# Kernel tuning notes

Measured on AMD Instinct MI355X. Metric: run time of the kernel, lower is better.

The kernel has to match this reference:

```python
import jax, jax.numpy as jnp
import numpy as np
from jax import lax

# --- static dims (match init_kwargs) ---
B = 16
Y, M, WIN = 10, 12, 48          # input_years, months_per_year, num_windows_per_month
T = Y * M * WIN                  # 5760 encoder timesteps
DENC = 256                       # encoder hidden size
U = 128                          # att_single_dense_units (bahdanau dim)
A1, A2 = 64, 32                  # att_single_dense_1st/2nd
K = 8                            # monthly/yearly num_kernels
KS, MPOOL, YPOOL = 3, 2, 2       # kernel_size, pool sizes (strides=1, VALID)
AMY = 64                         # att_mon_year_dense_1st
RNN = 256                        # RNN_num_units
FDEC = 64                        # dec_input features
NOUT = 64                        # n_output_features
# conv/pool output sizes (VALID conv, VALID pool stride 1)
H1, W1 = WIN - KS + 1 - MPOOL + 1, U - KS + 1 - MPOOL + 1      # 45, 125
H2, W2 = H1 - KS + 1 - MPOOL + 1, W1 - KS + 1 - MPOOL + 1      # 42, 122
FLATM = H2 * W2 * K                                            # 40992
HY, WY = M * H1 - KS + 1 - YPOOL + 1, W1 - KS + 1 - YPOOL + 1  # 537, 122
FLATY = HY * WY * K                                            # 524112


def conv_tanh(x, k, b):
    # Keras Conv2D(valid, activation='tanh'), NHWC/HWIO
    y = lax.conv_general_dilated(x, k, (1, 1), 'VALID',
                                 dimension_numbers=('NHWC', 'HWIO', 'NHWC'))
    return jnp.tanh(y + b)


def maxpool(x, p):
    # MaxPooling2D(pool_size=p, strides=1, valid)
    return lax.reduce_window(x, -jnp.inf, lax.max, (1, p, p, 1), (1, 1, 1, 1), 'VALID')


def setup_inputs() -> dict:
    key = jax.random.key(0)
    ks = jax.random.split(key, 24)
    r = lambda i, shape, s=0.02: jax.random.normal(ks[i], shape, jnp.float32) * s
    return {
        'dec_input': jax.random.normal(ks[0], (B, 1, FDEC), jnp.float32),
        'S_prev_dec': jax.random.normal(ks[1], (B, RNN), jnp.float32),
        'C_prev_dec': jax.random.normal(ks[2], (B, RNN), jnp.float32),
        'h_enc': jax.random.normal(ks[3], (B, T, DENC), jnp.float32),
        # attention_single params (all use_bias=False)
        'W_enc': r(4, (DENC, U)), 'W_dec': r(5, (RNN, U)),
        'W_att1': r(6, (U, A1)), 'W_att2': r(7, (A1, A2)), 'W_att3': r(8, (A2, 1)),
        # conv_pool layers
        'conv1_k': r(9, (KS, KS, 1, K)), 'conv1_b': jnp.zeros((K,), jnp.float32),
        'conv2_k': r(10, (KS, KS, K, K)), 'conv2_b': jnp.zeros((K,), jnp.float32),
        'convy_k': r(11, (KS, KS, K, K)), 'convy_b': jnp.zeros((K,), jnp.float32),
        # monthly / yearly attention denses (use_bias=True)
        'Wm1': r(12, (FLATM, AMY)), 'bm1': jnp.zeros((AMY,), jnp.float32),
        'Wm2': r(13, (AMY, 1)), 'bm2': jnp.zeros((1,), jnp.float32),
        'Wy1': r(14, (FLATY, AMY)), 'by1': jnp.zeros((AMY,), jnp.float32),
        'Wy2': r(15, (AMY, 1)), 'by2': jnp.zeros((1,), jnp.float32),
        # LSTM (input dim = DENC + FDEC); gate order i,f,g,o as in Keras
        'W_lstm': r(16, (DENC + FDEC, 4 * RNN)), 'U_lstm': r(17, (RNN, 4 * RNN)),
        'b_lstm': jnp.zeros((4 * RNN,), jnp.float32),
        # output dense
        'W_out': r(18, (RNN, NOUT)), 'b_out': jnp.zeros((NOUT,), jnp.float32),
    }


def reference(dec_input, S_prev_dec, C_prev_dec, h_enc,
              W_enc, W_dec, W_att1, W_att2, W_att3,
              conv1_k, conv1_b, conv2_k, conv2_b, convy_k, convy_b,
              Wm1, bm1, Wm2, bm2, Wy1, by1, Wy2, by2,
              W_lstm, U_lstm, b_lstm, W_out, b_out):
    # --- Bahdanau additive attention over all T encoder steps ---
    bah = h_enc @ W_enc + (S_prev_dec @ W_dec)[:, None, :]          # [B,T,U]
    e = jax.nn.relu(jax.nn.relu(jnp.tanh(bah @ W_att1) @ W_att2) @ W_att3)  # [B,T,1]
    aw = jax.nn.softmax(e, axis=1)[..., 0]                          # [B,T]
    # --- monthly conv-pool attention, batched over all Y*M month slices ---
    x = bah.reshape(B * Y * M, WIN, U, 1)
    c1 = maxpool(conv_tanh(x, conv1_k, conv1_b), MPOOL)             # [BYM,H1,W1,K]
    c2 = maxpool(conv_tanh(c1, conv2_k, conv2_b), MPOOL)            # [BYM,H2,W2,K]
    em = jax.nn.relu(jnp.tanh(c2.reshape(B * Y * M, FLATM) @ Wm1 + bm1) @ Wm2 + bm2)
    m_att = jax.nn.softmax(em.reshape(B, Y, M), axis=2)             # softmax over months
    # --- yearly conv-pool attention (months concatenated along height) ---
    yin = c1.reshape(B * Y, M * H1, W1, K)
    cy = maxpool(conv_tanh(yin, convy_k, convy_b), YPOOL)           # [BY,HY,WY,K]
    ey = jax.nn.relu(jnp.tanh(cy.reshape(B * Y, FLATY) @ Wy1 + by1) @ Wy2 + by2)
    y_att = jax.nn.softmax(ey.reshape(B, Y), axis=1)                # softmax over years
    # --- hierarchical combination of weights ---
    new_w = (aw.reshape(B, Y, M, WIN) * m_att[..., None]
             * y_att[:, :, None, None]).reshape(B, T)               # [B,T]
    ctx = jnp.einsum('bt,btd->bd', new_w, h_enc)                    # context [B,DENC]
    # --- single LSTM step on [context ; dec_input] ---
    xt = jnp.concatenate([ctx[:, None, :], dec_input], axis=-1)[:, 0, :]
    z = xt @ W_lstm + S_prev_dec @ U_lstm + b_lstm
    i, f, g, o = jnp.split(z, 4, axis=-1)
    c_new = jax.nn.sigmoid(f) * C_prev_dec + jax.nn.sigmoid(i) * jnp.tanh(g)
    h_new = jax.nn.sigmoid(o) * jnp.tanh(c_new)
    out = jax.nn.relu(h_new[:, None, :] @ W_out + b_out)            # [B,1,NOUT]
    return out, h_new, c_new, new_w
```

## Files before the change

### kernel.cpp

```cpp
#include <hip/hip_runtime.h>
#include <hip/hip_bf16.h>

#define DEV static __device__ __forceinline__

#define B_    16
#define Y_    10
#define M_    12
#define WIN_  48
#define T_    5760
#define DENC_ 256
#define U_    128
#define A1_   64
#define A2_   32
#define K_    8
#define RNN_  256
#define FDEC_ 64
#define NOUT_ 64

#define H1_   45
#define W1_   125
#define H2_   42
#define W2_   122
#define FLATM_ 40992
#define HY_   537
#define WY_   122
#define FLATY_ 524112
#define NSM_  1920
#define NSY_  160

typedef __attribute__((ext_vector_type(8))) short s16x8;
typedef __attribute__((ext_vector_type(4))) short s16x4;
typedef __attribute__((ext_vector_type(4))) float f32x4;

DEV float rcpf(float x){ return __builtin_amdgcn_rcpf(x); }
DEV float tanh_fast(float x){
  x = fminf(fmaxf(x, -15.0f), 15.0f);
  float e = __expf(2.0f*x);
  return 1.0f - 2.0f*rcpf(e + 1.0f);
}
DEV float tanh_nc(float x){
  float e = __expf(2.0f*x);
  return 1.0f - 2.0f*rcpf(e + 1.0f);
}
DEV float sigm(float x){ return rcpf(1.0f + __expf(-x)); }
DEV float wredsum(float v){
  #pragma unroll
  for (int off=32; off; off>>=1) v += __shfl_xor(v, off, 64);
  return v;
}
DEV short f2b(float f){
  __hip_bfloat16 h = __float2bfloat16(f);
  return *reinterpret_cast<short*>(&h);
}
DEV float b2f(short s){
  unsigned int x = ((unsigned int)(unsigned short)s) << 16;
  return __uint_as_float(x);
}
DEV unsigned int cvt_pk_bf16(float lo, float hi){
  unsigned int r;
  asm("v_cvt_pk_bf16_f32 %0, %1, %2" : "=v"(r) : "v"(lo), "v"(hi));
  return r;
}
DEV unsigned int swz_xor1u(unsigned int v){
  return (unsigned int)__builtin_amdgcn_ds_swizzle((int)v, 0x041F);
}
DEV unsigned int permb(unsigned int hi_src, unsigned int lo_src, unsigned int sel){
  return __builtin_amdgcn_perm(hi_src, lo_src, sel);
}

__global__ void k_cvt_bf16(const float* __restrict__ src, short* __restrict__ dst, long n4){
  long i = (long)blockIdx.x*256 + threadIdx.x;
  if (i < n4){
    f32x4 v = *(const f32x4*)(src + i*4);
    s16x4 o;
    #pragma unroll
    for (int q=0;q<4;q++) o[q] = f2b(v[q]);
    *(s16x4*)(dst + i*4) = o;
  }
}

__global__ void k_sdec(const float* __restrict__ S, const float* __restrict__ Wd,
                       float* __restrict__ sdec){
  int b = blockIdx.x, u = threadIdx.x;
  const float* s = S + b*DENC_;
  float acc = 0.f;
  #pragma unroll 4
  for (int d=0; d<DENC_; d++) acc += s[d]*Wd[d*U_+u];
  sdec[b*U_+u] = acc;
}

__global__ __launch_bounds__(256)
void k_bah_mfma(const float* __restrict__ h_enc, const short* __restrict__ Wenc_bf,
                const float* __restrict__ sdec, short* __restrict__ bah16){
  __shared__ short Wl[128*136];
  int tid = threadIdx.x;
  int m0 = blockIdx.x * 64;
  int lane = tid & 63, wid = tid >> 6;
  int pl = lane & 15, g = lane >> 4;
  long arow = m0 + wid*16 + pl;
  const float* ap = h_enc + arow*DENC_;
  f32x4 acc[8];
  #pragma unroll
  for (int i=0;i<8;i++) acc[i] = (f32x4){0.f,0.f,0.f,0.f};

  for (int kh=0; kh<2; kh++){
    for (int i=tid; i<16384; i+=256){
      int k = i >> 7, c = i & 127;
      Wl[c*136 + k] = Wenc_bf[(kh*128 + k)*U_ + c];
    }
    __syncthreads();
    #pragma unroll
    for (int kk=0; kk<4; kk++){
      f32x4 a0 = *(const f32x4*)(ap + kh*128 + kk*32 + g*8);
      f32x4 a1 = *(const f32x4*)(ap + kh*128 + kk*32 + g*8 + 4);
      s16x8 a;
      #pragma unroll
      for (int q=0;q<4;q++){ a[q] = f2b(a0[q]); a[4+q] = f2b(a1[q]); }
      #pragma unroll
      for (int nt=0; nt<8; nt++){
        s16x8 b = *(const s16x8*)(Wl + (nt*16+pl)*136 + kk*32 + g*8);
        acc[nt] = __builtin_amdgcn_mfma_f32_16x16x32_bf16(a, b, acc[nt], 0,0,0);
      }
    }
    __syncthreads();
  }
  int b = m0 / T_;
  #pragma unroll
  for (int nt=0; nt<8; nt++){
    float sd = sdec[b*U_ + nt*16 + pl];
    #pragma unroll
    for (int q=0; q<4; q++){
      long r = m0 + wid*16 + g*4 + q;
      bah16[r*U_ + nt*16 + pl] = f2b(acc[nt][q] + sd);
    }
  }
}

__global__ __launch_bounds__(256)
void k_att_mfma(const short* __restrict__ bah16, const float* __restrict__ W1,
                const float* __restrict__ W2, const float* __restrict__ W3f,
                float* __restrict__ e_out){
  __shared__ short W1l[64*136];
  __shared__ short W2l[32*72];
  __shared__ float hl[64][68];
  __shared__ float w3s[32];
  int tid = threadIdx.x;
  int lane = tid & 63, wid = tid >> 6;
  int pl = lane & 15, g = lane >> 4;
  long m0 = (long)blockIdx.x * 64;

  for (int i=tid; i<8192; i+=256){ int k=i>>6, c=i&63; W1l[c*136+k] = f2b(W1[k*64+c]); }
  for (int i=tid; i<2048; i+=256){ int k=i>>5, c=i&31; W2l[c*72+k]  = f2b(W2[k*32+c]); }
  if (tid < 32) w3s[tid] = W3f[tid];
  __syncthreads();

  const short* Ab = bah16 + (m0 + wid*16 + pl)*U_;
  f32x4 acc1[4];
  #pragma unroll
  for (int i=0;i<4;i++) acc1[i]=(f32x4){0.f,0.f,0.f,0.f};
  #pragma unroll
  for (int kk=0; kk<4; kk++){
    s16x8 a = *(const s16x8*)(Ab + kk*32 + g*8);
    #pragma unroll
    for (int nt=0; nt<4; nt++){
      s16x8 b = *(const s16x8*)(&W1l[(nt*16+pl)*136 + kk*32 + g*8]);
      acc1[nt] = __builtin_amdgcn_mfma_f32_16x16x32_bf16(a, b, acc1[nt], 0,0,0);
    }
  }
  #pragma unroll
  for (int nt=0; nt<4; nt++)
    #pragma unroll
    for (int q=0; q<4; q++)
      hl[wid*16 + g*4 + q][nt*16 + pl] = tanh_fast(acc1[nt][q]);
  __syncthreads();

  f32x4 acc2[2];
  #pragma unroll
  for (int i=0;i<2;i++) acc2[i]=(f32x4){0.f,0.f,0.f,0.f};
  #pragma unroll
  for (int kk=0; kk<2; kk++){
    f32x4 h0 = *(const f32x4*)(&hl[wid*16+pl][kk*32 + g*8]);
    f32x4 h1 = *(const f32x4*)(&hl[wid*16+pl][kk*32 + g*8 + 4]);
    s16x8 a;
    #pragma unroll
    for (int q=0;q<4;q++){ a[q]=f2b(h0[q]); a[4+q]=f2b(h1[q]); }
    #pragma unroll
    for (int nt=0; nt<2; nt++){
      s16x8 b = *(const s16x8*)(&W2l[(nt*16+pl)*72 + kk*32 + g*8]);
      acc2[nt] = __builtin_amdgcn_mfma_f32_16x16x32_bf16(a, b, acc2[nt], 0,0,0);
    }
  }
  #pragma unroll
  for (int q=0; q<4; q++){
    float v = fmaxf(acc2[0][q],0.f)*w3s[pl] + fmaxf(acc2[1][q],0.f)*w3s[16+pl];
    #pragma unroll
    for (int off=1; off<16; off<<=1) v += __shfl_xor(v, off, 64);
    if (pl == 0) e_out[m0 + wid*16 + g*4 + q] = fmaxf(v, 0.f);
  }
}

__global__ __launch_bounds__(256)
void k_softmax(const float* __restrict__ e, float* __restrict__ aw){
  int b = blockIdx.x, tid = threadIdx.x;
  __shared__ float red[4];
  const float* eb = e + (long)b*T_;
  float m = -1e30f;
  for (int t=tid; t<T_; t+=256) m = fmaxf(m, eb[t]);
  #pragma unroll
  for (int off=32; off; off>>=1) m = fmaxf(m, __shfl_xor(m, off, 64));
  if ((tid&63)==0) red[tid>>6] = m;
  __syncthreads();
  m = fmaxf(fmaxf(red[0],red[1]), fmaxf(red[2],red[3]));
  __syncthreads();
  float s = 0.f;
  for (int t=tid; t<T_; t+=256) s += __expf(eb[t]-m);
  s = wredsum(s);
  if ((tid&63)==0) red[tid>>6] = s;
  __syncthreads();
  s = red[0]+red[1]+red[2]+red[3];
  float inv = 1.0f/s;
  float* awb = aw + (long)b*T_;
  for (int t=tid; t<T_; t+=256) awb[t] = __expf(eb[t]-m)*inv;
}

__global__ __launch_bounds__(256)
void k_conv1s(const short* __restrict__ bah16, const float* __restrict__ k1,
              const float* __restrict__ b1, short* __restrict__ c1){
  int n = blockIdx.x >> 1, s = blockIdx.x & 1;
  int rp0 = s ? 23 : 0;
  int rp1 = s ? 44 : 22;
  int nin = rp1 + 4 - rp0;
  int tid = threadIdx.x;
  int lane = tid & 63, wid = tid >> 6;
  int c  = lane & 7;
  int wb = wid*8 + (lane >> 3);
  __shared__ float x[26][132];
  const short* xb = bah16 + (long)n*48*128 + rp0*128;
  for (int i=tid; i<nin*128; i+=256) x[i>>7][i&127] = b2f(xb[i]);
  for (int i=tid; i<26*4; i+=256)   x[i>>2][128+(i&3)] = 0.f;
  __syncthreads();

  float wk[9];
  #pragma unroll
  for (int p=0; p<9; p++) wk[p] = k1[p*8 + c];
  float bo = b1[c];
  bool odd = (c & 1);
  int qa = odd ? 2 : 0;
  bool va = (4*wb + qa)     <= 124;
  bool vb = (4*wb + qa + 1) <= 124;

  float rA[7], rB[7], rC[7];
  auto ldrow = [&](int rr, float* d){
    f32x4 a  = *(const f32x4*)(&x[rr][4*wb]);
    f32x4 b4 = *(const f32x4*)(&x[rr][4*wb+4]);
    d[0]=a[0]; d[1]=a[1]; d[2]=a[2]; d[3]=a[3]; d[4]=b4[0]; d[5]=b4[1]; d[6]=b4[2];
  };
  ldrow(0, rA); ldrow(1, rB);
  short* ob = c1 + (long)n*45*1000 + (long)rp0*1000;
  float vpc[4] = {0.f,0.f,0.f,0.f};
  int ncr = rp1 - rp0 + 2;

  for (int rr=0; rr<ncr; ++rr){
    ldrow(rr+2, rC);
    float cv[5];
    #pragma unroll
    for (int q=0; q<5; q++){
      cv[q] = bo + rA[q]*wk[0] + rA[q+1]*wk[1] + rA[q+2]*wk[2]
                 + rB[q]*wk[3] + rB[q+1]*wk[4] + rB[q+2]*wk[5]
                 + rC[q]*wk[6] + rC[q+1]*wk[7] + rC[q+2]*wk[8];
    }
    float wcv[4];
    #pragma unroll
    for (int q=0; q<4; q++) wcv[q] = fmaxf(cv[q], cv[q+1]);
    if (rr > 0){
      float t0 = tanh_nc(fmaxf(vpc[0], wcv[0]));
      float t1 = tanh_nc(fmaxf(vpc[1], wcv[1]));
      float t2 = tanh_nc(fmaxf(vpc[2], wcv[2]));
      float t3 = tanh_nc(fmaxf(vpc[3], wcv[3]));
      unsigned int A  = cvt_pk_bf16(t0, t1);
      unsigned int Bp = cvt_pk_bf16(t2, t3);
      unsigned int An = swz_xor1u(A);
      unsigned int Bn = swz_xor1u(Bp);
      unsigned int ph = odd ? Bp : An;
      unsigned int pw = odd ? Bn : A;
      unsigned int w0 = permb(ph, pw, 0x05040100u);
      unsigned int w1 = permb(ph, pw, 0x07060302u);
      long rbase = (long)(rr-1)*1000 + (c & ~1);
      if (va) *(unsigned int*)(ob + rbase + (4*wb+qa)*8)   = w0;
      if (vb) *(unsigned int*)(ob + rbase + (4*wb+qa+1)*8) = w1;
    }
    #pragma unroll
    for (int q=0; q<4; q++) vpc[q] = wcv[q];
    #pragma unroll
    for (int q=0; q<7; q++){ rA[q]=rB[q]; rB[q]=rC[q]; }
  }
}

#define LOADF(SL, OFF) { fa[SL] = *(const s16x8*)(gp + (OFF)); \
                         fb[SL] = *(const s16x8*)(gp + (OFF) + 128); }
#define CONVROW(SA,SB,SC, A0, A1) {                                          \
    A0 = (f32x4){0.f,0.f,0.f,0.f}; A1 = A0;                                  \
    A0 = __builtin_amdgcn_mfma_f32_16x16x32_bf16(fa[SA], bw[0], A0,0,0,0);   \
    A0 = __builtin_amdgcn_mfma_f32_16x16x32_bf16(fa[SB], bw[1], A0,0,0,0);   \
    A0 = __builtin_amdgcn_mfma_f32_16x16x32_bf16(fa[SC], bw[2], A0,0,0,0);   \
    A1 = __builtin_amdgcn_mfma_f32_16x16x32_bf16(fb[SA], bw[0], A1,0,0,0);   \
    A1 = __builtin_amdgcn_mfma_f32_16x16x32_bf16(fb[SB], bw[1], A1,0,0,0);   \
    A1 = __builtin_amdgcn_mfma_f32_16x16x32_bf16(fb[SC], bw[2], A1,0,0,0); }
#define PHASE(P) {                                                           \
    int ldr_ = base + (P) + 3; if (ldr_ > pmax_in) ldr_ = pmax_in;           \
    LOADF(((P)+3)&3, (long)(ldr_ - base)*1000);                              \
    f32x4 a0_, a1_;                                                          \
    CONVROW((P)&3, ((P)+1)&3, ((P)+2)&3, a0_, a1_);                          \
    epi(a0_, a1_, opg + (P)*976, base + (P));                                \
  }

__global__ __launch_bounds__(256)
void k_convf(const short* __restrict__ c1,
             const float* __restrict__ k2, const float* __restrict__ b2,
             const float* __restrict__ ky, const float* __restrict__ by,
             short* __restrict__ c2m, short* __restrict__ cy){
  int s  = blockIdx.x & 1;
  int nm = blockIdx.x >> 1;
  int n = nm / 12, m = nm % 12;
  int tid = threadIdx.x, lane = tid & 63, wid = tid >> 6;
  int pl = lane & 15, g = lane >> 4;
  bool isY = (pl >= 8);
  int ch = pl & 7;
  bool odd = (ch & 1);

  int rl_end = (m < 11) ? 45 : 42;
  int ps0 = s ? 23 : 0;
  int p1  = s ? rl_end : 23;
  int pmax_in = p1 + 2;

  const float* kern = isY ? ky : k2;
  s16x8 bw[3];
  #pragma unroll
  for (int dy=0; dy<3; dy++){
    #pragma unroll
    for (int i=0; i<8; i++){
      int k = g*8 + i;
      bw[dy][i] = (k < 24) ? f2b(kern[(dy*24 + k)*8 + ch]) : (short)0;
    }
  }
  float bo = isY ? by[ch] : b2[ch];

  int Tw = 31*wid;
  int qa = odd ? 2 : 0;
  int s0off = (Tw + g*4 + qa)*8 + (ch & ~1);
  bool v1a = (Tw + 16 + g*4 + qa)     <= 121;
  bool v1b = ((Tw + 16 + g*4 + qa + 1) <= 121) && !(odd && g == 3);
  int bpa16 = ((lane+16)&63)*4;
  int bpaPL = pl*4;

  const short* gp = c1 + ((long)n*540 + 45*m + ps0)*1000 + (size_t)((Tw + pl + g)*8);
  short* opg = isY ? (cy  + ((long)n*537 + (long)45*m + ps0 - 1)*976)
                   : (c2m + ((long)(n*12+m)*42 + ps0 - 1)*976);

  s16x8 fa[4], fb[4];
  LOADF(0, 0);
  LOADF(1, 1000);
  LOADF(2, 2000);

  float vp[8];
  #pragma unroll
  for (int i=0;i<8;i++) vp[i]=0.f;

  auto epi = [&](const f32x4& a0, const f32x4& a1, short* rowptr, int row){
    float n0 = __int_as_float(__builtin_amdgcn_ds_bpermute(bpa16, __float_as_int(a0[0])));
    float n1 = __int_as_float(__builtin_amdgcn_ds_bpermute(bpa16, __float_as_int(a1[0])));
    float nbv = __int_as_float(__builtin_amdgcn_ds_bpermute(bpaPL, __float_as_int(a1[0])));
    float nxt0 = (g < 3) ? n0 : nbv;
    float w[8];
    w[0]=fmaxf(a0[0],a0[1]); w[1]=fmaxf(a0[1],a0[2]);
    w[2]=fmaxf(a0[2],a0[3]); w[3]=fmaxf(a0[3],nxt0);
    w[4]=fmaxf(a1[0],a1[1]); w[5]=fmaxf(a1[1],a1[2]);
    w[6]=fmaxf(a1[2],a1[3]); w[7]=fmaxf(a1[3],n1);
    bool en = (row > ps0) && (isY || row <= 42);
    if (en){
      float t0 = tanh_nc(fmaxf(vp[0], w[0]) + bo);
      float t1 = tanh_nc(fmaxf(vp[1], w[1]) + bo);
      float t2 = tanh_nc(fmaxf(vp[2], w[2]) + bo);
      float t3 = tanh_nc(fmaxf(vp[3], w[3]) + bo);
      float t4 = tanh_nc(fmaxf(vp[4], w[4]) + bo);
      float t5 = tanh_nc(fmaxf(vp[5], w[5]) + bo);
      float t6 = tanh_nc(fmaxf(vp[6], w[6]) + bo);
      float t7 = tanh_nc(fmaxf(vp[7], w[7]) + bo);
      unsigned int A  = cvt_pk_bf16(t0, t1);
      unsigned int Bp = cvt_pk_bf16(t2, t3);
      unsigned int An = swz_xor1u(A);
      unsigned int Bn = swz_xor1u(Bp);
      unsigned int ph = odd ? Bp : An;
      unsigned int pw = odd ? Bn : A;
      unsigned int d0 = permb(ph, pw, 0x05040100u);
      unsigned int d1 = permb(ph, pw, 0x07060302u);
      unsigned int C  = cvt_pk_bf16(t4, t5);
      unsigned int Dp = cvt_pk_bf16(t6, t7);
      unsigned int Cn = swz_xor1u(C);
      unsigned int Dn = swz_xor1u(Dp);
      unsigned int qh = odd ? Dp : Cn;
      unsigned int qw = odd ? Dn : C;
      unsigned int d2 = permb(qh, qw, 0x05040100u);
      unsigned int d3 = permb(qh, qw, 0x07060302u);
      *(unsigned int*)(rowptr + s0off)       = d0;
      *(unsigned int*)(rowptr + s0off + 8)   = d1;
      if (v1a) *(unsigned int*)(rowptr + s0off + 128) = d2;
      if (v1b) *(unsigned int*)(rowptr + s0off + 136) = d3;
    }
    #pragma unroll
    for (int i=0;i<8;i++) vp[i] = w[i];
  };

  int base = ps0;
  for (; base + 3 <= p1; base += 4){
    PHASE(0)
    PHASE(1)
    PHASE(2)
    PHASE(3)
    gp += 4000; opg += 4*976;
  }
  int rem = p1 - base + 1;
  if (rem > 0){ PHASE(0) }
  if (rem > 1){ PHASE(1) }
  if (rem > 2){ PHASE(2) }
}
#undef PHASE
#undef CONVROW
#undef LOADF

__global__ void k_init64(float* __restrict__ C, const float* __restrict__ bias, int n){
  int i = blockIdx.x*256 + threadIdx.x;
  if (i < n) C[i] = bias[i & 63];
}

__global__ __launch_bounds__(256)
void k_gemm64m(const __hip_bfloat16* __restrict__ A, const float* __restrict__ W,
               float* __restrict__ C, int Mrows, long Kdim, int mtiles, int spc){
  __shared__ short Ws_t[2][64*72];
  int mt = blockIdx.x % mtiles;
  int kc = blockIdx.x / mtiles;
  long nsteps = (Kdim + 63) >> 6;
  long s0 = (long)kc * spc;
  if (s0 >= nsteps) return;
  long s1 = min(nsteps, s0 + (long)spc);
  int m0 = mt * 64;
  int tid = threadIdx.x;
  int lane = tid & 63, wid = tid >> 6;
  int pl = lane & 15, g = lane >> 4;
  long arow = m0 + wid*16 + pl;
  if (arow >= Mrows) arow = 0;
  const short* Ab = (const short*)A + arow*Kdim;
  int wc = tid & 63, wk0 = (tid >> 6)*2;
  f32x4 acc[4];
  #pragma unroll
  for (int i=0;i<4;i++) acc[i]=(f32x4){0.f,0.f,0.f,0.f};

  float wr[16];
  auto loadW = [&](long s, float* w){
    long kb = s << 6;
    #pragma unroll
    for (int j=0;j<8;j++){
      long kg = kb + wk0 + j*8;
      w[2*j]   = (kg   < Kdim) ? W[kg*64 + wc]     : 0.f;
      w[2*j+1] = (kg+1 < Kdim) ? W[(kg+1)*64 + wc] : 0.f;
    }
  };
  auto writeW = [&](int buf, const float* w){
    #pragma unroll
    for (int j=0;j<8;j++){
      unsigned int p = cvt_pk_bf16(w[2*j], w[2*j+1]);
      *(unsigned int*)(&Ws_t[buf][wc*72 + wk0 + j*8]) = p;
    }
  };
  s16x8 aA[2], aN[2];
  auto loadA = [&](long s, s16x8* a){
    long kb = s << 6;
    #pragma unroll
    for (int kk=0;kk<2;kk++){
      long ko = kb + kk*32 + g*8;
      a[kk] = (ko < Kdim) ? *(const s16x8*)(Ab + ko) : (s16x8){0,0,0,0,0,0,0,0};
    }
  };

  loadW(s0, wr);
  loadA(s0, aA);
  writeW(0, wr);
  __syncthreads();
  int cur = 0;
  for (long s = s0; s < s1; ++s){
    bool more = (s+1 < s1);
    float wrn[16];
    if (more){ loadW(s+1, wrn); loadA(s+1, aN); }
    #pragma unroll
    for (int kk=0; kk<2; kk++){
      #pragma unroll
      for (int nt=0; nt<4; nt++){
        s16x8 b = *(const s16x8*)(&Ws_t[cur][(nt*16+pl)*72 + kk*32 + g*8]);
        acc[nt] = __builtin_amdgcn_mfma_f32_16x16x32_bf16(aA[kk], b, acc[nt], 0,0,0);
      }
    }
    if (more){
      __syncthreads();
      writeW(cur^1, wrn);
      __syncthreads();
      aA[0] = aN[0]; aA[1] = aN[1];
      cur ^= 1;
    }
  }
  #pragma unroll
  for (int nt=0; nt<4; nt++){
    #pragma unroll
    for (int q=0; q<4; q++){
      int r = m0 + wid*16 + g*4 + q;
      if (r < Mrows) atomicAdd(&C[(long)r*64 + nt*16 + pl], acc[nt][q]);
    }
  }
}

__global__ void k_month_head(const float* __restrict__ em_pre, const float* __restrict__ Wm2,
                             const float* __restrict__ bm2, float* __restrict__ m_att){
  int g = blockIdx.x;
  int tid = threadIdx.x;
  __shared__ float em[M_];
  float w2 = Wm2[tid];
  for (int m=0; m<M_; m++){
    float v = tanh_fast(em_pre[(g*M_+m)*64 + tid]) * w2;
    v = wredsum(v);
    if (tid==0) em[m] = fmaxf(v + bm2[0], 0.f);
  }
  __syncthreads();
  if (tid==0){
    float mx = -1e30f;
    for (int m=0;m<M_;m++) mx = fmaxf(mx, em[m]);
    float s=0.f; float ex[M_];
    for (int m=0;m<M_;m++){ ex[m]=__expf(em[m]-mx); s+=ex[m]; }
    float inv = 1.0f/s;
    for (int m=0;m<M_;m++) m_att[g*M_+m] = ex[m]*inv;
  }
}

__global__ void k_year_head(const float* __restrict__ ey_pre, const float* __restrict__ Wy2,
                            const float* __restrict__ by2, float* __restrict__ y_att){
  int b = blockIdx.x;
  int tid = threadIdx.x;
  __shared__ float ey[Y_];
  float w2 = Wy2[tid];
  for (int y=0; y<Y_; y++){
    float v = tanh_fast(ey_pre[(b*Y_+y)*64 + tid]) * w2;
    v = wredsum(v);
    if (tid==0) ey[y] = fmaxf(v + by2[0], 0.f);
  }
  __syncthreads();
  if (tid==0){
    float mx = -1e30f;
    for (int y=0;y<Y_;y++) mx = fmaxf(mx, ey[y]);
    float s=0.f; float ex[Y_];
    for (int y=0;y<Y_;y++){ ex[y]=__expf(ey[y]-mx); s+=ex[y]; }
    float inv = 1.0f/s;
    for (int y=0;y<Y_;y++) y_att[b*Y_+y] = ex[y]*inv;
  }
}

__global__ void k_new_w(const float* __restrict__ aw, const float* __restrict__ m_att,
                        const float* __restrict__ y_att, float* __restrict__ nw){
  int idx = blockIdx.x*256 + threadIdx.x;
  if (idx < B_*T_){
    int b = idx / T_, t = idx % T_;
    int y = t / (M_*WIN_), m = (t % (M_*WIN_)) / WIN_;
    nw[idx] = aw[idx] * m_att[(b*Y_+y)*M_+m] * y_att[b*Y_+y];
  }
}

__global__ void k_zero(float* __restrict__ p, int n){
  int i = blockIdx.x*256 + threadIdx.x; if (i<n) p[i]=0.f;
}

__global__ __launch_bounds__(256)
void k_ctx(const float* __restrict__ nw, const float* __restrict__ h_enc,
           float* __restrict__ ctx){
  int b = blockIdx.x >> 6, ch = blockIdx.x & 63;
  int d = threadIdx.x;
  float acc = 0.f;
  int t0 = ch*(T_/64), t1 = t0 + (T_/64);
  for (int t=t0; t<t1; t++)
    acc += nw[b*T_+t] * h_enc[((long)b*T_+t)*DENC_ + d];
  atomicAdd(&ctx[b*DENC_+d], acc);
}

__global__ void k_lstm_z(const float* __restrict__ ctx, const float* __restrict__ dec,
                         const float* __restrict__ S, const float* __restrict__ Wl,
                         const float* __restrict__ Ul, const float* __restrict__ bl,
                         float* __restrict__ z){
  int b = blockIdx.x >> 2;
  int j = (blockIdx.x & 3)*256 + threadIdx.x;
  float acc = bl[j];
  const float* cb = ctx + b*DENC_;
  const float* db = dec + b*FDEC_;
  const float* sb = S + b*RNN_;
  #pragma unroll 4
  for (int d=0; d<DENC_; d++) acc += cb[d]*Wl[d*1024 + j];
  #pragma unroll 4
  for (int d=0; d<FDEC_; d++) acc += db[d]*Wl[(DENC_+d)*1024 + j];
  #pragma unroll 4
  for (int d=0; d<RNN_; d++) acc += sb[d]*Ul[d*1024 + j];
  z[b*1024 + j] = acc;
}

__global__ void k_gates(const float* __restrict__ z, const float* __restrict__ Cprev,
                        float* __restrict__ h_out, float* __restrict__ c_out){
  int b = blockIdx.x, j = threadIdx.x;
  const float* zb = z + b*1024;
  float iv = sigm(zb[j]);
  float fv = sigm(zb[256+j]);
  float gv = tanh_fast(zb[512+j]);
  float ov = sigm(zb[768+j]);
  float c = fv*Cprev[b*RNN_+j] + iv*gv;
  float h = ov*tanh_fast(c);
  h_out[b*RNN_+j] = h;
  c_out[b*RNN_+j] = c;
}

__global__ void k_out(const float* __restrict__ h, const float* __restrict__ Wo,
                      const float* __restrict__ bo, float* __restrict__ out){
  int b = blockIdx.x, q = threadIdx.x;
  float acc = bo[q];
  #pragma unroll 4
  for (int j=0; j<RNN_; j++) acc += h[b*RNN_+j]*Wo[j*64+q];
  out[b*64+q] = fmaxf(acc, 0.f);
}

extern "C" void kernel_launch(void* const* d_in, const int* in_sizes, int n_in,
                              void* d_out, int out_size, void* d_ws, size_t ws_size,
                              hipStream_t stream){
  const float* dec_input = (const float*)d_in[0];
  const float* S_prev = (const float*)d_in[1];
  const float* C_prev = (const float*)d_in[2];
  const float* h_enc  = (const float*)d_in[3];
  const float* W_enc  = (const float*)d_in[4];
  const float* W_dec  = (const float*)d_in[5];
  const float* W_att1 = (const float*)d_in[6];
  const float* W_att2 = (const float*)d_in[7];
  const float* W_att3 = (const float*)d_in[8];
  const float* conv1_k= (const float*)d_in[9];
  const float* conv1_b= (const float*)d_in[10];
  const float* conv2_k= (const float*)d_in[11];
  const float* conv2_b= (const float*)d_in[12];
  const float* convy_k= (const float*)d_in[13];
  const float* convy_b= (const float*)d_in[14];
  const float* Wm1    = (const float*)d_in[15];
  const float* bm1    = (const float*)d_in[16];
  const float* Wm2    = (const float*)d_in[17];
  const float* bm2    = (const float*)d_in[18];
  const float* Wy1    = (const float*)d_in[19];
  const float* by1    = (const float*)d_in[20];
  const float* Wy2    = (const float*)d_in[21];
  const float* by2    = (const float*)d_in[22];
  const float* W_lstm = (const float*)d_in[23];
  const float* U_lstm = (const float*)d_in[24];
  const float* b_lstm = (const float*)d_in[25];
  const float* W_out  = (const float*)d_in[26];
  const float* b_out  = (const float*)d_in[27];

  char* ws = (char*)d_ws;
  size_t off = 0;
  auto alloc = [&](size_t bytes)->char*{
    char* p = ws + off; off += (bytes + 255) & ~(size_t)255; return p;
  };
  short* bah16          = (short*)alloc((size_t)B_*T_*U_*2);
  short* c1             = (short*)alloc((size_t)NSM_*H1_*W1_*K_*2);
  short* c2m            = (short*)alloc((size_t)NSM_*H2_*W2_*K_*2);
  short* cy             = (short*)alloc((size_t)NSY_*HY_*WY_*K_*2);
  float* e              = (float*)alloc((size_t)B_*T_*4);
  float* aw             = (float*)alloc((size_t)B_*T_*4);
  float* sdec           = (float*)alloc(B_*U_*4);
  float* em_pre         = (float*)alloc(NSM_*64*4);
  float* ey_pre         = (float*)alloc(NSY_*64*4);
  float* m_att          = (float*)alloc(NSM_*4);
  float* y_att          = (float*)alloc(NSY_*4);
  float* ctx            = (float*)alloc(B_*DENC_*4);
  float* zbuf           = (float*)alloc(B_*1024*4);
  short* Wenc_bf        = (short*)alloc(DENC_*U_*2);

  float* out   = (float*)d_out;
  float* h_new = out + 1024;
  float* c_new = h_new + 4096;
  float* nw    = c_new + 4096;

  k_cvt_bf16<<<(DENC_*U_/4 + 255)/256, 256, 0, stream>>>(W_enc, Wenc_bf, DENC_*U_/4);
  k_sdec<<<B_, U_, 0, stream>>>(S_prev, W_dec, sdec);
  k_bah_mfma<<<(B_*T_)/64, 256, 0, stream>>>(h_enc, Wenc_bf, sdec, bah16);
  k_att_mfma<<<(B_*T_)/64, 256, 0, stream>>>(bah16, W_att1, W_att2, W_att3, e);
  k_softmax<<<B_, 256, 0, stream>>>(e, aw);
  k_conv1s<<<NSM_*2, 256, 0, stream>>>(bah16, conv1_k, conv1_b, c1);
  k_convf<<<NSY_*12*2, 256, 0, stream>>>(c1, conv2_k, conv2_b, convy_k, convy_b, c2m, cy);
  k_init64<<<(NSM_*64+255)/256, 256, 0, stream>>>(em_pre, bm1, NSM_*64);
  k_gemm64m<<<81*30, 256, 0, stream>>>((const __hip_bfloat16*)c2m, Wm1, em_pre, NSM_, (long)FLATM_, 30, 8);
  k_month_head<<<NSY_, 64, 0, stream>>>(em_pre, Wm2, bm2, m_att);
  k_init64<<<(NSY_*64+255)/256, 256, 0, stream>>>(ey_pre, by1, NSY_*64);
  k_gemm64m<<<512*3, 256, 0, stream>>>((const __hip_bfloat16*)cy, Wy1, ey_pre, NSY_, (long)FLATY_, 3, 16);
  k_year_head<<<B_, 64, 0, stream>>>(ey_pre, Wy2, by2, y_att);
  k_new_w<<<(B_*T_+255)/256, 256, 0, stream>>>(aw, m_att, y_att, nw);
  k_zero<<<(B_*DENC_+255)/256, 256, 0, stream>>>(ctx, B_*DENC_);
  k_ctx<<<B_*64, 256, 0, stream>>>(nw, h_enc, ctx);
  k_lstm_z<<<B_*4, 256, 0, stream>>>(ctx, dec_input, S_prev, W_lstm, U_lstm, b_lstm, zbuf);
  k_gates<<<B_, 256, 0, stream>>>(zbuf, C_prev, h_new, c_new);
  k_out<<<B_, 64, 0, stream>>>(h_new, W_out, b_out, out);
}
```

Measured before the change: 621.6 us.

## Fuse Bahdanau projection with attention MLP and merge small setup kernels

Merges the bf16 weight conversion, decoder projection, bias initialisations and ctx zeroing into a single multi-role setup kernel, which removes several tiny launches. Fuses the encoder projection GEMM with the attention MLP so the bah tile stays in shared memory and no longer has to be read back from global memory. It also stores the tanh hidden layer as bf16 in LDS. The fused kernel uses more shared memory and may run at lower occupancy.

```diff
diff --git a/kernel.cpp b/kernel.cpp
--- a/kernel.cpp
+++ b/kernel.cpp
@@ -68,31 +68,55 @@
   return __builtin_amdgcn_perm(hi_src, lo_src, sel);
 }
 
-__global__ void k_cvt_bf16(const float* __restrict__ src, short* __restrict__ dst, long n4){
-  long i = (long)blockIdx.x*256 + threadIdx.x;
-  if (i < n4){
-    f32x4 v = *(const f32x4*)(src + i*4);
+__global__ __launch_bounds__(256)
+void k_setup(const float* __restrict__ W_enc, short* __restrict__ Wenc_bf,
+             const float* __restrict__ S, const float* __restrict__ Wd,
+             float* __restrict__ sdec,
+             const float* __restrict__ bm1, float* __restrict__ em_pre,
+             const float* __restrict__ by1, float* __restrict__ ey_pre,
+             float* __restrict__ ctx){
+  int blk = blockIdx.x, tid = threadIdx.x;
+  if (blk < 32){
+    int i = blk*256 + tid;
+    f32x4 v = *(const f32x4*)(W_enc + (long)i*4);
     s16x4 o;
     #pragma unroll
     for (int q=0;q<4;q++) o[q] = f2b(v[q]);
-    *(s16x4*)(dst + i*4) = o;
-  }
-}
-
-__global__ void k_sdec(const float* __restrict__ S, const float* __restrict__ Wd,
-                       float* __restrict__ sdec){
-  int b = blockIdx.x, u = threadIdx.x;
-  const float* s = S + b*DENC_;
-  float acc = 0.f;
-  #pragma unroll 4
-  for (int d=0; d<DENC_; d++) acc += s[d]*Wd[d*U_+u];
-  sdec[b*U_+u] = acc;
+    *(s16x4*)(Wenc_bf + (long)i*4) = o;
+  } else if (blk < 48){
+    int b = blk - 32;
+    if (tid < U_){
+      const float* s = S + b*DENC_;
+      float acc = 0.f;
+      #pragma unroll 4
+      for (int d=0; d<DENC_; d++) acc += s[d]*Wd[d*U_+tid];
+      sdec[b*U_+tid] = acc;
+    }
+  } else if (blk < 528){
+    int i = (blk-48)*256 + tid;
+    em_pre[i] = bm1[i & 63];
+  } else if (blk < 568){
+    int i = (blk-528)*256 + tid;
+    ey_pre[i] = by1[i & 63];
+  } else {
+    int i = (blk-568)*256 + tid;
+    ctx[i] = 0.f;
+  }
 }
 
 __global__ __launch_bounds__(256)
-void k_bah_mfma(const float* __restrict__ h_enc, const short* __restrict__ Wenc_bf,
-                const float* __restrict__ sdec, short* __restrict__ bah16){
-  __shared__ short Wl[128*136];
+void k_bah_att(const float* __restrict__ h_enc, const short* __restrict__ Wenc_bf,
+               const float* __restrict__ sdec,
+               const float* __restrict__ W1, const float* __restrict__ W2,
+               const float* __restrict__ W3f,
+               short* __restrict__ bah16, float* __restrict__ e_out){
+  __shared__ char smem[48768];
+  short* Wl   = (short*)smem;
+  short* bahl = (short*)smem;
+  short* W1l  = (short*)(smem + 17408);
+  short* W2l  = (short*)(smem + 34816);
+  short* hlb  = (short*)(smem + 39424);
+  float* w3s  = (float*)(smem + 48640);
   int tid = threadIdx.x;
   int m0 = blockIdx.x * 64;
   int lane = tid & 63, wid = tid >> 6;
@@ -129,49 +153,37 @@
   for (int nt=0; nt<8; nt++){
     float sd = sdec[b*U_ + nt*16 + pl];
     #pragma unroll
-    for (int q=0; q<4; q++){
-      long r = m0 + wid*16 + g*4 + q;
-      bah16[r*U_ + nt*16 + pl] = f2b(acc[nt][q] + sd);
-    }
-  }
-}
-
-__global__ __launch_bounds__(256)
-void k_att_mfma(const short* __restrict__ bah16, const float* __restrict__ W1,
-                const float* __restrict__ W2, const float* __restrict__ W3f,
-                float* __restrict__ e_out){
-  __shared__ short W1l[64*136];
-  __shared__ short W2l[32*72];
-  __shared__ float hl[64][68];
-  __shared__ float w3s[32];
-  int tid = threadIdx.x;
-  int lane = tid & 63, wid = tid >> 6;
-  int pl = lane & 15, g = lane >> 4;
-  long m0 = (long)blockIdx.x * 64;
-
+    for (int q=0; q<4; q++)
+      bahl[(wid*16 + g*4 + q)*136 + nt*16 + pl] = f2b(acc[nt][q] + sd);
+  }
   for (int i=tid; i<8192; i+=256){ int k=i>>6, c=i&63; W1l[c*136+k] = f2b(W1[k*64+c]); }
   for (int i=tid; i<2048; i+=256){ int k=i>>5, c=i&31; W2l[c*72+k]  = f2b(W2[k*32+c]); }
   if (tid < 32) w3s[tid] = W3f[tid];
   __syncthreads();
 
-  const short* Ab = bah16 + (m0 + wid*16 + pl)*U_;
+  for (int i=tid; i<1024; i+=256){
+    int r = i >> 4, cc = (i & 15)*8;
+    s16x8 v = *(const s16x8*)&bahl[r*136 + cc];
+    *(s16x8*)&bah16[(long)(m0 + r)*U_ + cc] = v;
+  }
+
   f32x4 acc1[4];
   #pragma unroll
   for (int i=0;i<4;i++) acc1[i]=(f32x4){0.f,0.f,0.f,0.f};
   #pragma unroll
   for (int kk=0; kk<4; kk++){
-    s16x8 a = *(const s16x8*)(Ab + kk*32 + g*8);
+    s16x8 a = *(const s16x8*)&bahl[(wid*16+pl)*136 + kk*32 + g*8];
     #pragma unroll
     for (int nt=0; nt<4; nt++){
-      s16x8 b = *(const s16x8*)(&W1l[(nt*16+pl)*136 + kk*32 + g*8]);
-      acc1[nt] = __builtin_amdgcn_mfma_f32_16x16x32_bf16(a, b, acc1[nt], 0,0,0);
+      s16x8 bb = *(const s16x8*)&W1l[(nt*16+pl)*136 + kk*32 + g*8];
+      acc1[nt] = __builtin_amdgcn_mfma_f32_16x16x32_bf16(a, bb, acc1[nt], 0,0,0);
     }
   }
   #pragma unroll
   for (int nt=0; nt<4; nt++)
     #pragma unroll
     for (int q=0; q<4; q++)
-      hl[wid*16 + g*4 + q][nt*16 + pl] = tanh_fast(acc1[nt][q]);
+      hlb[(wid*16 + g*4 + q)*72 + nt*16 + pl] = f2b(tanh_fast(acc1[nt][q]));
   __syncthreads();
 
   f32x4 acc2[2];
@@ -179,15 +191,11 @@
   for (int i=0;i<2;i++) acc2[i]=(f32x4){0.f,0.f,0.f,0.f};
   #pragma unroll
   for (int kk=0; kk<2; kk++){
-    f32x4 h0 = *(const f32x4*)(&hl[wid*16+pl][kk*32 + g*8]);
-    f32x4 h1 = *(const f32x4*)(&hl[wid*16+pl][kk*32 + g*8 + 4]);
-    s16x8 a;
-    #pragma unroll
-    for (int q=0;q<4;q++){ a[q]=f2b(h0[q]); a[4+q]=f2b(h1[q]); }
+    s16x8 a = *(const s16x8*)&hlb[(wid*16+pl)*72 + kk*32 + g*8];
     #pragma unroll
     for (int nt=0; nt<2; nt++){
-      s16x8 b = *(const s16x8*)(&W2l[(nt*16+pl)*72 + kk*32 + g*8]);
-      acc2[nt] = __builtin_amdgcn_mfma_f32_16x16x32_bf16(a, b, acc2[nt], 0,0,0);
+      s16x8 bb = *(const s16x8*)&W2l[(nt*16+pl)*72 + kk*32 + g*8];
+      acc2[nt] = __builtin_amdgcn_mfma_f32_16x16x32_bf16(a, bb, acc2[nt], 0,0,0);
     }
   }
   #pragma unroll
@@ -195,7 +203,7 @@
     float v = fmaxf(acc2[0][q],0.f)*w3s[pl] + fmaxf(acc2[1][q],0.f)*w3s[16+pl];
     #pragma unroll
     for (int off=1; off<16; off<<=1) v += __shfl_xor(v, off, 64);
-    if (pl == 0) e_out[m0 + wid*16 + g*4 + q] = fmaxf(v, 0.f);
+    if (pl == 0) e_out[(long)m0 + wid*16 + g*4 + q] = fmaxf(v, 0.f);
   }
 }
 
@@ -428,11 +436,6 @@
 #undef CONVROW
 #undef LOADF
 
-__global__ void k_init64(float* __restrict__ C, const float* __restrict__ bias, int n){
-  int i = blockIdx.x*256 + threadIdx.x;
-  if (i < n) C[i] = bias[i & 63];
-}
-
 __global__ __launch_bounds__(256)
 void k_gemm64m(const __hip_bfloat16* __restrict__ A, const float* __restrict__ W,
                float* __restrict__ C, int Mrows, long Kdim, int mtiles, int spc){
@@ -569,10 +572,6 @@
     int y = t / (M_*WIN_), m = (t % (M_*WIN_)) / WIN_;
     nw[idx] = aw[idx] * m_att[(b*Y_+y)*M_+m] * y_att[b*Y_+y];
   }
-}
-
-__global__ void k_zero(float* __restrict__ p, int n){
-  int i = blockIdx.x*256 + threadIdx.x; if (i<n) p[i]=0.f;
 }
 
 __global__ __launch_bounds__(256)
@@ -686,21 +685,18 @@
   float* c_new = h_new + 4096;
   float* nw    = c_new + 4096;
 
-  k_cvt_bf16<<<(DENC_*U_/4 + 255)/256, 256, 0, stream>>>(W_enc, Wenc_bf, DENC_*U_/4);
-  k_sdec<<<B_, U_, 0, stream>>>(S_prev, W_dec, sdec);
-  k_bah_mfma<<<(B_*T_)/64, 256, 0, stream>>>(h_enc, Wenc_bf, sdec, bah16);
-  k_att_mfma<<<(B_*T_)/64, 256, 0, stream>>>(bah16, W_att1, W_att2, W_att3, e);
+  k_setup<<<584, 256, 0, stream>>>(W_enc, Wenc_bf, S_prev, W_dec, sdec,
+                                   bm1, em_pre, by1, ey_pre, ctx);
+  k_bah_att<<<(B_*T_)/64, 256, 0, stream>>>(h_enc, Wenc_bf, sdec,
+                                            W_att1, W_att2, W_att3, bah16, e);
   k_softmax<<<B_, 256, 0, stream>>>(e, aw);
   k_conv1s<<<NSM_*2, 256, 0, stream>>>(bah16, conv1_k, conv1_b, c1);
   k_convf<<<NSY_*12*2, 256, 0, stream>>>(c1, conv2_k, conv2_b, convy_k, convy_b, c2m, cy);
-  k_init64<<<(NSM_*64+255)/256, 256, 0, stream>>>(em_pre, bm1, NSM_*64);
   k_gemm64m<<<81*30, 256, 0, stream>>>((const __hip_bfloat16*)c2m, Wm1, em_pre, NSM_, (long)FLATM_, 30, 8);
   k_month_head<<<NSY_, 64, 0, stream>>>(em_pre, Wm2, bm2, m_att);
-  k_init64<<<(NSY_*64+255)/256, 256, 0, stream>>>(ey_pre, by1, NSY_*64);
   k_gemm64m<<<512*3, 256, 0, stream>>>((const __hip_bfloat16*)cy, Wy1, ey_pre, NSY_, (long)FLATY_, 3, 16);
   k_year_head<<<B_, 64, 0, stream>>>(ey_pre, Wy2, by2, y_att);
   k_new_w<<<(B_*T_+255)/256, 256, 0, stream>>>(aw, m_att, y_att, nw);
-  k_zero<<<(B_*DENC_+255)/256, 256, 0, stream>>>(ctx, B_*DENC_);
   k_ctx<<<B_*64, 256, 0, stream>>>(nw, h_enc, ctx);
   k_lstm_z<<<B_*4, 256, 0, stream>>>(ctx, dec_input, S_prev, W_lstm, U_lstm, b_lstm, zbuf);
   k_gates<<<B_, 256, 0, stream>>>(zbuf, C_prev, h_new, c_new);
```

Measured after the change: 607.0 us. 2.3% less time.
